# Kernel optimization log

Measured on AMD Instinct MI355X. Metric: run time of the kernel, lower is better.

The kernel has to match this reference:

```python
import jax, jax.numpy as jnp
import numpy as np

B, T, C, H = 512, 4096, 7, 3  # batch, time, 7 classes, 3 heads


def setup_inputs() -> dict:
    key = jax.random.key(0)
    k0, k1, k2, k3, k4, k5 = jax.random.split(key, 6)
    # outputs are treated as probabilities (log is taken directly); keep them in (0.01, 1]
    mk_out = lambda k: jax.random.uniform(k, (B, T, C), dtype=jnp.float32, minval=0.01, maxval=1.0)
    return {
        "out0": mk_out(k0),
        "out1": mk_out(k1),
        "out2": mk_out(k2),
        "labels_3": jax.random.randint(k3, (B, T, H), 0, C, dtype=jnp.int64),
        "mask": jax.random.uniform(k4, (B, T), dtype=jnp.float32),
        "reward": jax.random.uniform(k5, (B, T, H), dtype=jnp.float32),
    }


def reference(out0, out1, out2, labels_3, mask, reward):
    N = B * T
    outs = jnp.stack([out0, out1, out2], axis=0).reshape(H, N, C)   # [3, N, 7]
    labels = labels_3.reshape(N, H).T                               # [3, N]
    rw = reward.reshape(N, H).T                                     # [3, N]
    valid = mask.reshape(N) < 0.5                                   # [N] bool
    n_valid = valid.sum()

    # gather probability of the true class per head: op[h, n] = outs[h, n, labels[h, n]]
    op = jnp.take_along_axis(outs, labels[:, :, None], axis=2)[..., 0]  # [3, N]
    # original: sum_h -dot(log(op_h), sr_h) / n_valid  (n_valid identical across heads)
    loss = -jnp.where(valid[None, :], jnp.log(op) * rw, 0.0).sum() / n_valid

    pred = jnp.argmax(outs, axis=-1)                                # [3, N]
    correct = jnp.all(pred == labels, axis=0) & valid               # product over heads on valid positions
    n_correct = correct.sum()
    return loss, n_correct, n_valid
```

## Files before the change

kernel.cpp:

```cpp
#include <hip/hip_runtime.h>

constexpr long long N_ROWS = 512LL * 4096LL;
constexpr int ROWS_PER_THREAD = 4;
constexpr int BLOCK = 256;
constexpr int NBLOCKS = (int)(N_ROWS / (long long)ROWS_PER_THREAD / BLOCK);


__global__ __launch_bounds__(BLOCK) void shortloss_main(
    const float* __restrict__ out0,
    const float* __restrict__ out1,
    const float* __restrict__ out2,
    const int*   __restrict__ labels,
    const float* __restrict__ mask,
    const float* __restrict__ reward,
    float4*      __restrict__ partials)
{
    const long long t    = (long long)blockIdx.x * BLOCK + threadIdx.x;
    const long long row0 = t * ROWS_PER_THREAD;

    float4 m4 = *reinterpret_cast<const float4*>(mask + row0);
    const float mm[4] = {m4.x, m4.y, m4.z, m4.w};
    bool valid[4];
    int  vcount = 0;
    #pragma unroll
    for (int r = 0; r < 4; ++r) { valid[r] = mm[r] < 0.5f; vcount += valid[r] ? 1 : 0; }

    int lab[12];
    {
        const int4* lp = reinterpret_cast<const int4*>(labels + row0 * 3);
        int4 a = lp[0], b = lp[1], c = lp[2];
        lab[0]=a.x; lab[1]=a.y; lab[2]=a.z;  lab[3]=a.w;
        lab[4]=b.x; lab[5]=b.y; lab[6]=b.z;  lab[7]=b.w;
        lab[8]=c.x; lab[9]=c.y; lab[10]=c.z; lab[11]=c.w;
    }

    float rw[12];
    {
        const float4* rp = reinterpret_cast<const float4*>(reward + row0 * 3);
        float4 a = rp[0], b = rp[1], c = rp[2];
        rw[0]=a.x; rw[1]=a.y; rw[2]=a.z;  rw[3]=a.w;
        rw[4]=b.x; rw[5]=b.y; rw[6]=b.z;  rw[7]=b.w;
        rw[8]=c.x; rw[9]=c.y; rw[10]=c.z; rw[11]=c.w;
    }

    float loss_local = 0.0f;
    bool  corr[4] = {true, true, true, true};

    const float* outs[3] = {out0, out1, out2};
    #pragma unroll
    for (int h = 0; h < 3; ++h) {
        const float4* op4 = reinterpret_cast<const float4*>(outs[h] + row0 * 7);
        float v[28];
        #pragma unroll
        for (int i = 0; i < 7; ++i) {
            float4 q = op4[i];
            v[4*i+0]=q.x; v[4*i+1]=q.y; v[4*i+2]=q.z; v[4*i+3]=q.w;
        }
        #pragma unroll
        for (int r = 0; r < 4; ++r) {
            const int lbl = lab[r*3 + h];
            float best  = v[r*7];
            int   bestc = 0;
            #pragma unroll
            for (int c = 1; c < 7; ++c) {
                float val = v[r*7 + c];
                if (val > best) { best = val; bestc = c; }
            }
            float opv = v[r*7];
            #pragma unroll
            for (int c = 1; c < 7; ++c) {
                opv = (lbl == c) ? v[r*7 + c] : opv;
            }
            loss_local += valid[r] ? __logf(opv) * rw[r*3 + h] : 0.0f;
            corr[r] = corr[r] && (bestc == lbl);
        }
    }

    int ccount = 0;
    #pragma unroll
    for (int r = 0; r < 4; ++r) ccount += (corr[r] && valid[r]) ? 1 : 0;

    #pragma unroll
    for (int off = 32; off > 0; off >>= 1) {
        loss_local += __shfl_down(loss_local, off, 64);
        ccount     += __shfl_down(ccount,     off, 64);
        vcount     += __shfl_down(vcount,     off, 64);
    }

    __shared__ float s_loss[BLOCK / 64];
    __shared__ int   s_c[BLOCK / 64];
    __shared__ int   s_v[BLOCK / 64];
    const int wave = threadIdx.x >> 6;
    if ((threadIdx.x & 63) == 0) {
        s_loss[wave] = loss_local;
        s_c[wave]    = ccount;
        s_v[wave]    = vcount;
    }
    __syncthreads();
    if (threadIdx.x == 0) {
        float L = 0.0f; int C = 0, V = 0;
        #pragma unroll
        for (int w = 0; w < BLOCK / 64; ++w) { L += s_loss[w]; C += s_c[w]; V += s_v[w]; }
        partials[blockIdx.x] = make_float4(L, (float)C, (float)V, 0.0f);
    }
}

__global__ __launch_bounds__(256) void shortloss_reduce(
    const float4* __restrict__ partials,
    float* __restrict__ out)
{
    float L = 0.0f, C = 0.0f, V = 0.0f;
    for (int i = threadIdx.x; i < NBLOCKS; i += 256) {
        float4 p = partials[i];
        L += p.x; C += p.y; V += p.z;
    }
    #pragma unroll
    for (int off = 32; off > 0; off >>= 1) {
        L += __shfl_down(L, off, 64);
        C += __shfl_down(C, off, 64);
        V += __shfl_down(V, off, 64);
    }
    __shared__ float sL[4], sC[4], sV[4];
    const int wave = threadIdx.x >> 6;
    if ((threadIdx.x & 63) == 0) { sL[wave] = L; sC[wave] = C; sV[wave] = V; }
    __syncthreads();
    if (threadIdx.x == 0) {
        float l = 0.0f, c = 0.0f, v = 0.0f;
        #pragma unroll
        for (int w = 0; w < 4; ++w) { l += sL[w]; c += sC[w]; v += sV[w]; }
        out[0] = -l / v;
        out[1] = c;
        out[2] = v;
    }
}

extern "C" void kernel_launch(void* const* d_in, const int* in_sizes, int n_in,
                              void* d_out, int out_size, void* d_ws, size_t ws_size,
                              hipStream_t stream) {
    const float* out0   = (const float*)d_in[0];
    const float* out1   = (const float*)d_in[1];
    const float* out2   = (const float*)d_in[2];
    const int*   labels = (const int*)  d_in[3];
    const float* mask   = (const float*)d_in[4];
    const float* reward = (const float*)d_in[5];

    float4* partials = (float4*)d_ws;

    shortloss_main<<<NBLOCKS, BLOCK, 0, stream>>>(
        out0, out1, out2, labels, mask, reward, partials);
    shortloss_reduce<<<1, 256, 0, stream>>>(partials, (float*)d_out);
}
```

Before: 228.7 us.

## Stage inputs through LDS with direct global-to-LDS loads over grid-strided chunks

Replaces the per-thread four-row vector loads with a fixed grid of 2048 blocks. Each block loops over 256-row chunks and uses global_load_lds 16-byte async copies to stage outputs, labels, reward and mask into LDS with fully coalesced, contiguous accesses. Each thread then processes one row from LDS. This targets the poorly coalesced 112-byte-strided per-lane global reads of the old kernel. In exchange there is no double buffering, so every chunk pays a barrier-to-barrier load latency. The 28 KB of LDS per block also limits how many blocks can be resident per CU, which may reduce memory-level parallelism.

```diff
diff --git a/kernel.cpp b/kernel.cpp
--- a/kernel.cpp
+++ b/kernel.cpp
@@ -1,10 +1,19 @@
 #include <hip/hip_runtime.h>
 
 constexpr long long N_ROWS = 512LL * 4096LL;
-constexpr int ROWS_PER_THREAD = 4;
-constexpr int BLOCK = 256;
-constexpr int NBLOCKS = (int)(N_ROWS / (long long)ROWS_PER_THREAD / BLOCK);
+constexpr int BLOCK  = 256;
+constexpr int CHUNK  = 256;
+constexpr int NBLOCKS = 2048;
+constexpr int NCHUNKS_TOTAL   = (int)(N_ROWS / CHUNK);
+constexpr int CHUNKS_PER_BLOCK = NCHUNKS_TOTAL / NBLOCKS;
 
+
+__device__ __forceinline__ void async_copy16(const void* g, void* l) {
+    __builtin_amdgcn_global_load_lds(
+        (const __attribute__((address_space(1))) unsigned int*)g,
+        (__attribute__((address_space(3))) unsigned int*)l,
+        16, 0, 0);
+}
 
 __global__ __launch_bounds__(BLOCK) void shortloss_main(
     const float* __restrict__ out0,
@@ -15,93 +24,96 @@
     const float* __restrict__ reward,
     float4*      __restrict__ partials)
 {
-    const long long t    = (long long)blockIdx.x * BLOCK + threadIdx.x;
-    const long long row0 = t * ROWS_PER_THREAD;
+    __shared__ float lds[7168];
+    float* lds_out = lds;
+    int*   lds_lab = (int*)(lds + 5376);
+    float* lds_rw  = lds + 6144;
+    float* lds_msk = lds + 6912;
 
-    float4 m4 = *reinterpret_cast<const float4*>(mask + row0);
-    const float mm[4] = {m4.x, m4.y, m4.z, m4.w};
-    bool valid[4];
-    int  vcount = 0;
-    #pragma unroll
-    for (int r = 0; r < 4; ++r) { valid[r] = mm[r] < 0.5f; vcount += valid[r] ? 1 : 0; }
+    const int tid = threadIdx.x;
+    const float* outs[3] = {out0, out1, out2};
 
-    int lab[12];
-    {
-        const int4* lp = reinterpret_cast<const int4*>(labels + row0 * 3);
-        int4 a = lp[0], b = lp[1], c = lp[2];
-        lab[0]=a.x; lab[1]=a.y; lab[2]=a.z;  lab[3]=a.w;
-        lab[4]=b.x; lab[5]=b.y; lab[6]=b.z;  lab[7]=b.w;
-        lab[8]=c.x; lab[9]=c.y; lab[10]=c.z; lab[11]=c.w;
+    float loss_local = 0.0f;
+    int   ccount = 0, vcount = 0;
+
+    for (int k = 0; k < CHUNKS_PER_BLOCK; ++k) {
+        const long long c    = (long long)k * NBLOCKS + blockIdx.x;
+        const long long row0 = c * CHUNK;
+
+        #pragma unroll
+        for (int h = 0; h < 3; ++h) {
+            const float* src = outs[h] + row0 * 7;
+            float*       dst = lds_out + h * 1792;
+            async_copy16(src + (size_t)tid * 4, dst + tid * 4);
+            if (tid < 192)
+                async_copy16(src + (size_t)(256 + tid) * 4, dst + (256 + tid) * 4);
+        }
+        if (tid < 192) {
+            async_copy16(labels + row0 * 3 + (size_t)tid * 4, lds_lab + tid * 4);
+            async_copy16(reward + row0 * 3 + (size_t)tid * 4, lds_rw  + tid * 4);
+        }
+        if (tid < 64) {
+            async_copy16(mask + row0 + (size_t)tid * 4, lds_msk + tid * 4);
+        }
+        __syncthreads();
+
+        const bool valid = lds_msk[tid] < 0.5f;
+        vcount += valid ? 1 : 0;
+
+        int lab[3], h_ok = 1;
+        float rw[3];
+        #pragma unroll
+        for (int h = 0; h < 3; ++h) {
+            lab[h] = lds_lab[tid * 3 + h];
+            rw[h]  = lds_rw [tid * 3 + h];
+        }
+
+        float lsum = 0.0f;
+        #pragma unroll
+        for (int h = 0; h < 3; ++h) {
+            const float* vr = lds_out + h * 1792 + tid * 7;
+            float v[7];
+            #pragma unroll
+            for (int cc = 0; cc < 7; ++cc) v[cc] = vr[cc];
+
+            float best = v[0]; int bestc = 0;
+            #pragma unroll
+            for (int cc = 1; cc < 7; ++cc)
+                if (v[cc] > best) { best = v[cc]; bestc = cc; }
+
+            float opv = v[0];
+            #pragma unroll
+            for (int cc = 1; cc < 7; ++cc)
+                opv = (lab[h] == cc) ? v[cc] : opv;
+
+            lsum += __logf(opv) * rw[h];
+            h_ok &= (bestc == lab[h]) ? 1 : 0;
+        }
+        loss_local += valid ? lsum : 0.0f;
+        ccount     += (valid && h_ok) ? 1 : 0;
+
+        __syncthreads();
     }
 
-    float rw[12];
-    {
-        const float4* rp = reinterpret_cast<const float4*>(reward + row0 * 3);
-        float4 a = rp[0], b = rp[1], c = rp[2];
-        rw[0]=a.x; rw[1]=a.y; rw[2]=a.z;  rw[3]=a.w;
-        rw[4]=b.x; rw[5]=b.y; rw[6]=b.z;  rw[7]=b.w;
-        rw[8]=c.x; rw[9]=c.y; rw[10]=c.z; rw[11]=c.w;
+    float L = loss_local;
+    int   C = ccount, V = vcount;
+    #pragma unroll
+    for (int off = 32; off > 0; off >>= 1) {
+        L += __shfl_down(L, off, 64);
+        C += __shfl_down(C, off, 64);
+        V += __shfl_down(V, off, 64);
     }
 
-    float loss_local = 0.0f;
-    bool  corr[4] = {true, true, true, true};
-
-    const float* outs[3] = {out0, out1, out2};
-    #pragma unroll
-    for (int h = 0; h < 3; ++h) {
-        const float4* op4 = reinterpret_cast<const float4*>(outs[h] + row0 * 7);
-        float v[28];
+    __shared__ float sL[BLOCK / 64];
+    __shared__ int   sC[BLOCK / 64], sV[BLOCK / 64];
+    const int wave = tid >> 6;
+    if ((tid & 63) == 0) { sL[wave] = L; sC[wave] = C; sV[wave] = V; }
+    __syncthreads();
+    if (tid == 0) {
+        float l = 0.0f; int cc = 0, vv = 0;
         #pragma unroll
-        for (int i = 0; i < 7; ++i) {
-            float4 q = op4[i];
-            v[4*i+0]=q.x; v[4*i+1]=q.y; v[4*i+2]=q.z; v[4*i+3]=q.w;
-        }
-        #pragma unroll
-        for (int r = 0; r < 4; ++r) {
-            const int lbl = lab[r*3 + h];
-            float best  = v[r*7];
-            int   bestc = 0;
-            #pragma unroll
-            for (int c = 1; c < 7; ++c) {
-                float val = v[r*7 + c];
-                if (val > best) { best = val; bestc = c; }
-            }
-            float opv = v[r*7];
-            #pragma unroll
-            for (int c = 1; c < 7; ++c) {
-                opv = (lbl == c) ? v[r*7 + c] : opv;
-            }
-            loss_local += valid[r] ? __logf(opv) * rw[r*3 + h] : 0.0f;
-            corr[r] = corr[r] && (bestc == lbl);
-        }
-    }
-
-    int ccount = 0;
-    #pragma unroll
-    for (int r = 0; r < 4; ++r) ccount += (corr[r] && valid[r]) ? 1 : 0;
-
-    #pragma unroll
-    for (int off = 32; off > 0; off >>= 1) {
-        loss_local += __shfl_down(loss_local, off, 64);
-        ccount     += __shfl_down(ccount,     off, 64);
-        vcount     += __shfl_down(vcount,     off, 64);
-    }
-
-    __shared__ float s_loss[BLOCK / 64];
-    __shared__ int   s_c[BLOCK / 64];
-    __shared__ int   s_v[BLOCK / 64];
-    const int wave = threadIdx.x >> 6;
-    if ((threadIdx.x & 63) == 0) {
-        s_loss[wave] = loss_local;
-        s_c[wave]    = ccount;
-        s_v[wave]    = vcount;
-    }
-    __syncthreads();
-    if (threadIdx.x == 0) {
-        float L = 0.0f; int C = 0, V = 0;
-        #pragma unroll
-        for (int w = 0; w < BLOCK / 64; ++w) { L += s_loss[w]; C += s_c[w]; V += s_v[w]; }
-        partials[blockIdx.x] = make_float4(L, (float)C, (float)V, 0.0f);
+        for (int w = 0; w < BLOCK / 64; ++w) { l += sL[w]; cc += sC[w]; vv += sV[w]; }
+        partials[blockIdx.x] = make_float4(l, (float)cc, (float)vv, 0.0f);
     }
 }
 
```

Result: no change. 227.7 us (-0.4%).
